# Kernel tuning notes

Measured on AMD Instinct MI355X. Metric: run time of the kernel, lower is better.

## Reference

```python
import jax, jax.numpy as jnp
import numpy as np

WS = (7, 7)        # window size
SHIFT = (3, 3)     # shift size
NUM_HEADS = 12


def _relative_position_index(ws):
    ch, cw = np.arange(ws[0]), np.arange(ws[1])
    coords = np.stack(np.meshgrid(ch, cw, indexing='ij'))          # [2, wh, ww]
    cf = coords.reshape(2, -1)                                     # [2, wh*ww]
    rel = cf[:, :, None] - cf[:, None, :]                          # [2, T, T]
    rel = rel.transpose(1, 2, 0)
    rel[:, :, 0] += ws[0] - 1
    rel[:, :, 1] += ws[1] - 1
    rel[:, :, 0] *= 2 * ws[1] - 1
    return rel.sum(-1)                                             # [T, T]


def _attn_mask(pad_H, pad_W, ws, shift):
    # static construction of the shifted-window mask (numpy, per torch code)
    img = np.zeros((pad_H, pad_W), dtype=np.float32)
    h_slices = ((0, pad_H - ws[0]), (pad_H - ws[0], pad_H - shift[0]), (pad_H - shift[0], pad_H))
    w_slices = ((0, pad_W - ws[1]), (pad_W - ws[1], pad_W - shift[1]), (pad_W - shift[1], pad_W))
    cnt = 0
    for h0, h1 in h_slices:
        for w0, w1 in w_slices:
            img[h0:h1, w0:w1] = cnt
            cnt += 1
    nW = (pad_H // ws[0]) * (pad_W // ws[1])
    m = img.reshape(pad_H // ws[0], ws[0], pad_W // ws[1], ws[1])
    m = m.transpose(0, 2, 1, 3).reshape(nW, ws[0] * ws[1])
    diff = m[:, None, :] - m[:, :, None]
    return np.where(diff != 0, -100.0, 0.0).astype(np.float32)     # [nW, T, T]


def setup_inputs() -> dict:
    key = jax.random.key(0)
    ks = jax.random.split(key, 6)
    dim = 384
    return {
        'x': jax.random.normal(ks[0], (32, 56, 56, dim), dtype=jnp.float32),
        'qkv_weight': jax.random.normal(ks[1], (3 * dim, dim), dtype=jnp.float32) * 0.02,
        'qkv_bias': jax.random.normal(ks[2], (3 * dim,), dtype=jnp.float32) * 0.02,
        'proj_weight': jax.random.normal(ks[3], (dim, dim), dtype=jnp.float32) * 0.02,
        'proj_bias': jax.random.normal(ks[4], (dim,), dtype=jnp.float32) * 0.02,
        'rel_pos_bias_table': jax.random.normal(ks[5], ((2 * WS[0] - 1) * (2 * WS[1] - 1), NUM_HEADS), dtype=jnp.float32) * 0.02,
    }


def reference(x, qkv_weight, qkv_bias, proj_weight, proj_bias, rel_pos_bias_table):
    B, H, W, C = x.shape
    wh, ww = WS
    T = wh * ww
    nh = NUM_HEADS
    dh = C // nh

    pad_b = (wh - H % wh) % wh
    pad_r = (ww - W % ww) % ww
    x = jnp.pad(x, ((0, 0), (0, pad_b), (0, pad_r), (0, 0)))
    pad_H, pad_W = H + pad_b, W + pad_r
    shift = [SHIFT[0] if wh < pad_H else 0, SHIFT[1] if ww < pad_W else 0]

    # relative position bias [1, nh, T, T]
    rpi = _relative_position_index(WS)                               # static int index
    bias = rel_pos_bias_table[jnp.asarray(rpi.reshape(-1))].reshape(T, T, nh)
    bias = jnp.transpose(bias, (2, 0, 1))[None]

    if sum(shift) > 0:
        x = jnp.roll(x, (-shift[0], -shift[1]), axis=(1, 2))

    nH, nW_ = pad_H // wh, pad_W // ww
    num_windows = nH * nW_
    # window partition -> [B*num_windows, T, C]
    xw = x.reshape(B, nH, wh, nW_, ww, C).transpose(0, 1, 3, 2, 4, 5).reshape(B * num_windows, T, C)

    qkv = xw @ qkv_weight.T + qkv_bias                               # [Bn, T, 3C]
    qkv = qkv.reshape(B * num_windows, T, 3, nh, dh).transpose(2, 0, 3, 1, 4)
    q, k, v = qkv[0], qkv[1], qkv[2]                                 # [Bn, nh, T, dh]

    attn = jnp.einsum('bhtd,bhsd->bhts', q * (dh ** -0.5), k) + bias

    if sum(shift) > 0:
        mask = jnp.asarray(_attn_mask(pad_H, pad_W, WS, shift))      # [nW, T, T]
        attn = attn.reshape(B, num_windows, nh, T, T) + mask[None, :, None]
        attn = attn.reshape(B * num_windows, nh, T, T)

    attn = jax.nn.softmax(attn, axis=-1)
    out = jnp.einsum('bhts,bhsd->bhtd', attn, v)                     # [Bn, nh, T, dh]
    out = out.transpose(0, 2, 1, 3).reshape(B * num_windows, T, C)
    out = out @ proj_weight.T + proj_bias

    out = out.reshape(B, nH, nW_, wh, ww, C).transpose(0, 1, 3, 2, 4, 5).reshape(B, pad_H, pad_W, C)
    if sum(shift) > 0:
        out = jnp.roll(out, (shift[0], shift[1]), axis=(1, 2))
    return out[:, :H, :W, :]
```

## Files before the change

### kernel.cpp

```cpp
#include <hip/hip_runtime.h>


typedef __bf16 bf16;
typedef __bf16 bf16x8 __attribute__((ext_vector_type(8)));
typedef __bf16 bf16x4 __attribute__((ext_vector_type(4)));
typedef float f32x4 __attribute__((ext_vector_type(4)));

#define NWIN   2048
#define WHN    24576
#define GTOK   100352
#define QKV_SCALE 0.17677669529663687f

#define QB_OFF 0u
#define KB_OFF 77070336u
#define VB_OFF 154140672u
#define XG_OFF 231211008u
#define BM_OFF 308281344u
#define WQ_OFF 314572800u
#define WP_OFF 315457536u

__device__ inline void gld16(const bf16* g, bf16* l) {
  __builtin_amdgcn_global_load_lds(
      (const __attribute__((address_space(1))) void*)g,
      (__attribute__((address_space(3))) void*)l, 16, 0, 0);
}

__global__ __launch_bounds__(256) void k_prep(
    const float* __restrict__ x, const float* __restrict__ wqkv,
    const float* __restrict__ wproj, const float* __restrict__ table,
    bf16* __restrict__ xg, bf16* __restrict__ wq, bf16* __restrict__ wp,
    bf16* __restrict__ bm) {
  int blk = blockIdx.x;
  if (blk < 18816) {
    int idx = blk * 256 + threadIdx.x;
    int g = idx / 48, cg = idx - g * 48;
    int w = g / 49, t = g - w * 49;
    int b = w >> 6, wi = w & 63;
    int wy = wi >> 3, wx = wi & 7;
    int ty = t / 7, tx = t - ty * 7;
    int sy = wy * 7 + ty + 3; if (sy >= 56) sy -= 56;
    int sx = wx * 7 + tx + 3; if (sx >= 56) sx -= 56;
    const float* src = x + (size_t)((b * 56 + sy) * 56 + sx) * 384 + cg * 8;
    float4 a0 = *(const float4*)src;
    float4 a1 = *(const float4*)(src + 4);
    bf16x8 o;
    o[0] = (bf16)a0.x; o[1] = (bf16)a0.y; o[2] = (bf16)a0.z; o[3] = (bf16)a0.w;
    o[4] = (bf16)a1.x; o[5] = (bf16)a1.y; o[6] = (bf16)a1.z; o[7] = (bf16)a1.w;
    *(bf16x8*)(xg + (size_t)g * 384 + cg * 8) = o;
  } else if (blk < 19104) {
    int idx = (blk - 18816) * 256 + threadIdx.x;
    const float* src; bf16* dst; int off;
    if (idx < 55296) { src = wqkv; dst = wq; off = idx * 8; }
    else             { src = wproj; dst = wp; off = (idx - 55296) * 8; }
    float4 a0 = *(const float4*)(src + off);
    float4 a1 = *(const float4*)(src + off + 4);
    bf16x8 o;
    o[0] = (bf16)a0.x; o[1] = (bf16)a0.y; o[2] = (bf16)a0.z; o[3] = (bf16)a0.w;
    o[4] = (bf16)a1.x; o[5] = (bf16)a1.y; o[6] = (bf16)a1.z; o[7] = (bf16)a1.w;
    *(bf16x8*)(dst + off) = o;
  } else {
    int idx = (blk - 19104) * 256 + threadIdx.x;
    int r = idx & 3;
    int lane = (idx >> 2) & 63;
    int c = (idx >> 8) & 3;
    int ts = (idx >> 10) & 3;
    int comb = idx >> 12;
    int h = comb % 12, wi = comb / 12;
    int i = ts * 16 + ((lane >> 4) << 2) + r;
    int j = c * 16 + (lane & 15);
    float v;
    if (j >= 49) v = -30000.f;
    else if (i >= 49) v = 0.f;
    else {
      int wy = wi >> 3, wx = wi & 7;
      int iy = i / 7, ix = i - iy * 7;
      int jy = j / 7, jx = j - jy * 7;
      int rel = (iy - jy + 6) * 13 + (ix - jx + 6);
      int gyi = wy * 7 + iy, gxi = wx * 7 + ix;
      int gyj = wy * 7 + jy, gxj = wx * 7 + jx;
      int ri = ((gyi < 49) ? 0 : ((gyi < 53) ? 1 : 2)) * 3 +
               ((gxi < 49) ? 0 : ((gxi < 53) ? 1 : 2));
      int rj = ((gyj < 49) ? 0 : ((gyj < 53) ? 1 : 2)) * 3 +
               ((gxj < 49) ? 0 : ((gxj < 53) ? 1 : 2));
      v = table[rel * 12 + h] + ((ri == rj) ? 0.f : -100.f);
    }
    bm[idx] = (bf16)v;
  }
}

__global__ __launch_bounds__(256, 3) void k_qkv(
    const bf16* __restrict__ xg, const bf16* __restrict__ wg,
    const float* __restrict__ bqkv, bf16* __restrict__ qb,
    bf16* __restrict__ kb, bf16* __restrict__ vb) {
  __shared__ __align__(16) bf16 As[128 * 64];
  __shared__ __align__(16) bf16 Bs[128 * 64];

  int tid = threadIdx.x;
  int wv = tid >> 6, lane = tid & 63, l16 = lane & 15, q4 = lane >> 4;
  int wr = wv >> 1, wc = wv & 1;
  int bid = blockIdx.x;
  int xcd = bid & 7, s = bid >> 3;
  int nb = s % 9, mt = s / 9;
  int m0 = (mt * 8 + xcd) * 128;
  int n0 = nb * 128;

  int srow = lane >> 3;
  int scg = lane & 7;

  f32x4 acc[4][4];
#pragma unroll
  for (int a = 0; a < 4; ++a)
#pragma unroll
    for (int b = 0; b < 4; ++b) acc[a][b] = (f32x4){0.f, 0.f, 0.f, 0.f};

  for (int k0 = 0; k0 < 384; k0 += 64) {
    __syncthreads();
#pragma unroll
    for (int st = 0; st < 4; ++st) {
      int row = (wv * 4 + st) * 8 + srow;
      int gc = (scg ^ (row & 7)) * 8;
      gld16(xg + (size_t)(m0 + row) * 384 + k0 + gc, As + (wv * 4 + st) * 512);
      gld16(wg + (size_t)(n0 + row) * 384 + k0 + gc, Bs + (wv * 4 + st) * 512);
    }
    __syncthreads();
#pragma unroll
    for (int kk = 0; kk < 2; ++kk) {
      bf16x8 af[4], bfr[4];
#pragma unroll
      for (int mi = 0; mi < 4; ++mi) {
        int m = wr * 64 + mi * 16 + l16;
        int g = kk * 4 + q4;
        af[mi] = *(const bf16x8*)(As + m * 64 + ((g ^ (m & 7)) * 8));
      }
#pragma unroll
      for (int ci = 0; ci < 4; ++ci) {
        int n = wc * 64 + ci * 16 + l16;
        int g = kk * 4 + q4;
        bfr[ci] = *(const bf16x8*)(Bs + n * 64 + ((g ^ (n & 7)) * 8));
      }
#pragma unroll
      for (int mi = 0; mi < 4; ++mi)
#pragma unroll
        for (int ci = 0; ci < 4; ++ci)
          acc[mi][ci] =
              __builtin_amdgcn_mfma_f32_16x16x32_bf16(af[mi], bfr[ci], acc[mi][ci], 0, 0, 0);
    }
  }

  int which = nb / 3;
  float bias4[4]; int h4[4], d4[4];
#pragma unroll
  for (int ci = 0; ci < 4; ++ci) {
    int n = n0 + wc * 64 + ci * 16 + l16;
    bias4[ci] = bqkv[n];
    int hd = n - which * 384;
    h4[ci] = hd >> 5; d4[ci] = hd & 31;
  }
#pragma unroll
  for (int mi = 0; mi < 4; ++mi) {
#pragma unroll
    for (int r = 0; r < 4; ++r) {
      int mrow = m0 + wr * 64 + mi * 16 + q4 * 4 + r;
      int w = mrow / 49, tt = mrow - w * 49;
      int wb = w * 12;
#pragma unroll
      for (int ci = 0; ci < 4; ++ci) {
        float val = acc[mi][ci][r] + bias4[ci];
        size_t addr = (size_t)((wb + h4[ci]) * 49 + tt) * 32 + d4[ci];
        if (which == 0)
          qb[addr] = (bf16)(val * QKV_SCALE);
        else if (which == 1)
          kb[addr] = (bf16)val;
        else
          vb[addr] = (bf16)val;
      }
    }
  }
}

__global__ __launch_bounds__(256) void k_attn(
    const bf16* __restrict__ qb, const bf16* __restrict__ kb,
    const bf16* __restrict__ vb, const bf16* __restrict__ bm,
    bf16* __restrict__ ab) {
  __shared__ __align__(16) bf16 P[4][16][72];

  int tid = threadIdx.x;
  int wv = tid >> 6, lane = tid & 63, l16 = lane & 15, q4 = lane >> 4;
  int whi = blockIdx.x * 4 + wv;
  int w = whi / 12, h = whi - w * 12;
  int wi = w & 63;

  const bf16* qq = qb + (size_t)whi * 1568;
  const bf16* kk = kb + (size_t)whi * 1568;
  const bf16* vv = vb + (size_t)whi * 1568;
  const bf16* bmb = bm + ((size_t)(wi * 12 + h) << 12);

  bf16x8 kf[4];
#pragma unroll
  for (int c = 0; c < 4; ++c)
    kf[c] = *(const bf16x8*)(kk + (c * 16 + l16) * 32 + q4 * 8);

  bf16x8 vf[2][2];
#pragma unroll
  for (int half = 0; half < 2; ++half)
#pragma unroll
    for (int c2 = 0; c2 < 2; ++c2)
#pragma unroll
      for (int j = 0; j < 8; ++j)
        vf[half][c2][j] = vv[(half * 32 + q4 * 8 + j) * 32 + c2 * 16 + l16];

  const f32x4 zero4 = {0.f, 0.f, 0.f, 0.f};

  for (int ts = 0; ts < 4; ++ts) {
    bf16x8 qf = *(const bf16x8*)(qq + (ts * 16 + l16) * 32 + q4 * 8);
    f32x4 s[4];
#pragma unroll
    for (int c = 0; c < 4; ++c)
      s[c] = __builtin_amdgcn_mfma_f32_16x16x32_bf16(qf, kf[c], zero4, 0, 0, 0);
#pragma unroll
    for (int c = 0; c < 4; ++c) {
      bf16x4 bv = *(const bf16x4*)(bmb + (ts * 4 + c) * 256 + lane * 4);
#pragma unroll
      for (int r = 0; r < 4; ++r) s[c][r] += (float)bv[r];
    }
#pragma unroll
    for (int r = 0; r < 4; ++r) {
      float m = fmaxf(fmaxf(s[0][r], s[1][r]), fmaxf(s[2][r], s[3][r]));
      m = fmaxf(m, __shfl_xor(m, 1));
      m = fmaxf(m, __shfl_xor(m, 2));
      m = fmaxf(m, __shfl_xor(m, 4));
      m = fmaxf(m, __shfl_xor(m, 8));
      float e0 = __expf(s[0][r] - m);
      float e1 = __expf(s[1][r] - m);
      float e2 = __expf(s[2][r] - m);
      float e3 = __expf(s[3][r] - m);
      float sm = e0 + e1 + e2 + e3;
      sm += __shfl_xor(sm, 1);
      sm += __shfl_xor(sm, 2);
      sm += __shfl_xor(sm, 4);
      sm += __shfl_xor(sm, 8);
      float inv = 1.0f / sm;
      int ir = q4 * 4 + r;
      P[wv][ir][l16] = (bf16)(e0 * inv);
      P[wv][ir][16 + l16] = (bf16)(e1 * inv);
      P[wv][ir][32 + l16] = (bf16)(e2 * inv);
      P[wv][ir][48 + l16] = (bf16)(e3 * inv);
    }
    __builtin_amdgcn_wave_barrier();
    bf16x8 p0 = *(const bf16x8*)&P[wv][l16][q4 * 8];
    bf16x8 p1 = *(const bf16x8*)&P[wv][l16][32 + q4 * 8];
    f32x4 o0 = __builtin_amdgcn_mfma_f32_16x16x32_bf16(p0, vf[0][0], zero4, 0, 0, 0);
    o0 = __builtin_amdgcn_mfma_f32_16x16x32_bf16(p1, vf[1][0], o0, 0, 0, 0);
    f32x4 o1 = __builtin_amdgcn_mfma_f32_16x16x32_bf16(p0, vf[0][1], zero4, 0, 0, 0);
    o1 = __builtin_amdgcn_mfma_f32_16x16x32_bf16(p1, vf[1][1], o1, 0, 0, 0);
    __builtin_amdgcn_wave_barrier();
#pragma unroll
    for (int r = 0; r < 4; ++r) {
      int i = ts * 16 + q4 * 4 + r;
      if (i < 49) {
        bf16* dst = ab + (size_t)(w * 49 + i) * 384 + h * 32;
        dst[l16] = (bf16)o0[r];
        dst[16 + l16] = (bf16)o1[r];
      }
    }
  }
}

__global__ __launch_bounds__(256, 3) void k_proj(
    const bf16* __restrict__ ab, const bf16* __restrict__ wp,
    const float* __restrict__ bp, float* __restrict__ out) {
  __shared__ __align__(16) bf16 As[128 * 64];
  __shared__ __align__(16) bf16 Bs[128 * 64];

  int tid = threadIdx.x;
  int wv = tid >> 6, lane = tid & 63, l16 = lane & 15, q4 = lane >> 4;
  int wr = wv >> 1, wc = wv & 1;
  int bid = blockIdx.x;
  int xcd = bid & 7, s = bid >> 3;
  int nb = s % 3, mt = s / 3;
  int m0 = (mt * 8 + xcd) * 128;
  int n0 = nb * 128;

  int srow = lane >> 3;
  int scg = lane & 7;

  f32x4 acc[4][4];
#pragma unroll
  for (int a = 0; a < 4; ++a)
#pragma unroll
    for (int b = 0; b < 4; ++b) acc[a][b] = (f32x4){0.f, 0.f, 0.f, 0.f};

  for (int k0 = 0; k0 < 384; k0 += 64) {
    __syncthreads();
#pragma unroll
    for (int st = 0; st < 4; ++st) {
      int row = (wv * 4 + st) * 8 + srow;
      int gc = (scg ^ (row & 7)) * 8;
      gld16(ab + (size_t)(m0 + row) * 384 + k0 + gc, As + (wv * 4 + st) * 512);
      gld16(wp + (size_t)(n0 + row) * 384 + k0 + gc, Bs + (wv * 4 + st) * 512);
    }
    __syncthreads();
#pragma unroll
    for (int kk = 0; kk < 2; ++kk) {
      bf16x8 af[4], bfr[4];
#pragma unroll
      for (int mi = 0; mi < 4; ++mi) {
        int m = wr * 64 + mi * 16 + l16;
        int g = kk * 4 + q4;
        af[mi] = *(const bf16x8*)(As + m * 64 + ((g ^ (m & 7)) * 8));
      }
#pragma unroll
      for (int ci = 0; ci < 4; ++ci) {
        int n = wc * 64 + ci * 16 + l16;
        int g = kk * 4 + q4;
        bfr[ci] = *(const bf16x8*)(Bs + n * 64 + ((g ^ (n & 7)) * 8));
      }
#pragma unroll
      for (int mi = 0; mi < 4; ++mi)
#pragma unroll
        for (int ci = 0; ci < 4; ++ci)
          acc[mi][ci] =
              __builtin_amdgcn_mfma_f32_16x16x32_bf16(af[mi], bfr[ci], acc[mi][ci], 0, 0, 0);
    }
  }

  float bias4[4]; int col4[4];
#pragma unroll
  for (int ci = 0; ci < 4; ++ci) {
    col4[ci] = n0 + wc * 64 + ci * 16 + l16;
    bias4[ci] = bp[col4[ci]];
  }
#pragma unroll
  for (int mi = 0; mi < 4; ++mi) {
#pragma unroll
    for (int r = 0; r < 4; ++r) {
      int mrow = m0 + wr * 64 + mi * 16 + q4 * 4 + r;
      int w = mrow / 49, t = mrow - w * 49;
      int b = w >> 6, wi = w & 63;
      int wy = wi >> 3, wx = wi & 7;
      int ty = t / 7, tx = t - ty * 7;
      int gy = wy * 7 + ty + 3; if (gy >= 56) gy -= 56;
      int gx = wx * 7 + tx + 3; if (gx >= 56) gx -= 56;
      float* orow = out + (size_t)((b * 56 + gy) * 56 + gx) * 384;
#pragma unroll
      for (int ci = 0; ci < 4; ++ci) orow[col4[ci]] = acc[mi][ci][r] + bias4[ci];
    }
  }
}

extern "C" void kernel_launch(void* const* d_in, const int* in_sizes, int n_in,
                              void* d_out, int out_size, void* d_ws,
                              size_t ws_size, hipStream_t stream) {
  const float* x     = (const float*)d_in[0];
  const float* wqkv  = (const float*)d_in[1];
  const float* bqkv  = (const float*)d_in[2];
  const float* wproj = (const float*)d_in[3];
  const float* bproj = (const float*)d_in[4];
  const float* table = (const float*)d_in[5];
  float* out = (float*)d_out;

  char* ws = (char*)d_ws;
  bf16* qb  = (bf16*)(ws + QB_OFF);
  bf16* kb  = (bf16*)(ws + KB_OFF);
  bf16* vb  = (bf16*)(ws + VB_OFF);
  bf16* xg  = (bf16*)(ws + XG_OFF);
  bf16* ab  = (bf16*)(ws + XG_OFF);
  bf16* bmb = (bf16*)(ws + BM_OFF);
  bf16* wqg = (bf16*)(ws + WQ_OFF);
  bf16* wpg = (bf16*)(ws + WP_OFF);

  k_prep<<<dim3(31392), dim3(256), 0, stream>>>(x, wqkv, wproj, table,
                                                xg, wqg, wpg, bmb);
  k_qkv<<<dim3(7056), dim3(256), 0, stream>>>(xg, wqg, bqkv, qb, kb, vb);
  k_attn<<<dim3(6144), dim3(256), 0, stream>>>(qb, kb, vb, bmb, ab);
  k_proj<<<dim3(2352), dim3(256), 0, stream>>>(ab, wpg, bproj, out);
}
```

Before: 526.7 us.

## Fuse QKV GEMM, window attention and projection into one per-window kernel

Replaces the three kernels for the QKV GEMM, attention and projection with a single kernel that processes one window per block. The padded 64-token window input is staged in LDS, and per-head Q/K/V and the attention output stay on chip, so the large Q/K/V and attention-output round trips through global memory disappear. The prep kernel now pads each window to 64 rows with zeros. In exchange each block uses about 120KB of LDS (occupancy 1), reads weights directly from global/L2 without LDS tiling, and does GEMM work on 15 padding rows per window.

```diff
diff --git a/kernel.cpp b/kernel.cpp
--- a/kernel.cpp
+++ b/kernel.cpp
@@ -6,18 +6,12 @@
 typedef __bf16 bf16x4 __attribute__((ext_vector_type(4)));
 typedef float f32x4 __attribute__((ext_vector_type(4)));
 
-#define NWIN   2048
-#define WHN    24576
-#define GTOK   100352
 #define QKV_SCALE 0.17677669529663687f
 
-#define QB_OFF 0u
-#define KB_OFF 77070336u
-#define VB_OFF 154140672u
-#define XG_OFF 231211008u
-#define BM_OFF 308281344u
-#define WQ_OFF 314572800u
-#define WP_OFF 315457536u
+#define XG_OFF 0u
+#define BM_OFF 100663296u
+#define WQ_OFF 106954752u
+#define WP_OFF 107839488u
 
 __device__ inline void gld16(const bf16* g, bf16* l) {
   __builtin_amdgcn_global_load_lds(
@@ -31,24 +25,28 @@
     bf16* __restrict__ xg, bf16* __restrict__ wq, bf16* __restrict__ wp,
     bf16* __restrict__ bm) {
   int blk = blockIdx.x;
-  if (blk < 18816) {
+  if (blk < 24576) {
     int idx = blk * 256 + threadIdx.x;
     int g = idx / 48, cg = idx - g * 48;
-    int w = g / 49, t = g - w * 49;
-    int b = w >> 6, wi = w & 63;
-    int wy = wi >> 3, wx = wi & 7;
-    int ty = t / 7, tx = t - ty * 7;
-    int sy = wy * 7 + ty + 3; if (sy >= 56) sy -= 56;
-    int sx = wx * 7 + tx + 3; if (sx >= 56) sx -= 56;
-    const float* src = x + (size_t)((b * 56 + sy) * 56 + sx) * 384 + cg * 8;
-    float4 a0 = *(const float4*)src;
-    float4 a1 = *(const float4*)(src + 4);
+    int w = g >> 6, t = g & 63;
     bf16x8 o;
-    o[0] = (bf16)a0.x; o[1] = (bf16)a0.y; o[2] = (bf16)a0.z; o[3] = (bf16)a0.w;
-    o[4] = (bf16)a1.x; o[5] = (bf16)a1.y; o[6] = (bf16)a1.z; o[7] = (bf16)a1.w;
+#pragma unroll
+    for (int j = 0; j < 8; ++j) o[j] = (bf16)0.f;
+    if (t < 49) {
+      int b = w >> 6, wi = w & 63;
+      int wy = wi >> 3, wx = wi & 7;
+      int ty = t / 7, tx = t - ty * 7;
+      int sy = wy * 7 + ty + 3; if (sy >= 56) sy -= 56;
+      int sx = wx * 7 + tx + 3; if (sx >= 56) sx -= 56;
+      const float* src = x + (size_t)((b * 56 + sy) * 56 + sx) * 384 + cg * 8;
+      float4 a0 = *(const float4*)src;
+      float4 a1 = *(const float4*)(src + 4);
+      o[0] = (bf16)a0.x; o[1] = (bf16)a0.y; o[2] = (bf16)a0.z; o[3] = (bf16)a0.w;
+      o[4] = (bf16)a1.x; o[5] = (bf16)a1.y; o[6] = (bf16)a1.z; o[7] = (bf16)a1.w;
+    }
     *(bf16x8*)(xg + (size_t)g * 384 + cg * 8) = o;
-  } else if (blk < 19104) {
-    int idx = (blk - 18816) * 256 + threadIdx.x;
+  } else if (blk < 24864) {
+    int idx = (blk - 24576) * 256 + threadIdx.x;
     const float* src; bf16* dst; int off;
     if (idx < 55296) { src = wqkv; dst = wq; off = idx * 8; }
     else             { src = wproj; dst = wp; off = (idx - 55296) * 8; }
@@ -59,7 +57,7 @@
     o[4] = (bf16)a1.x; o[5] = (bf16)a1.y; o[6] = (bf16)a1.z; o[7] = (bf16)a1.w;
     *(bf16x8*)(dst + off) = o;
   } else {
-    int idx = (blk - 19104) * 256 + threadIdx.x;
+    int idx = (blk - 24864) * 256 + threadIdx.x;
     int r = idx & 3;
     int lane = (idx >> 2) & 63;
     int c = (idx >> 8) & 3;
@@ -88,262 +86,214 @@
   }
 }
 
-__global__ __launch_bounds__(256, 3) void k_qkv(
-    const bf16* __restrict__ xg, const bf16* __restrict__ wg,
-    const float* __restrict__ bqkv, bf16* __restrict__ qb,
-    bf16* __restrict__ kb, bf16* __restrict__ vb) {
-  __shared__ __align__(16) bf16 As[128 * 64];
-  __shared__ __align__(16) bf16 Bs[128 * 64];
+__global__ __launch_bounds__(256, 1) void k_fused(
+    const bf16* __restrict__ xg, const bf16* __restrict__ wq,
+    const float* __restrict__ bqkv, const bf16* __restrict__ bm,
+    const bf16* __restrict__ wp, const float* __restrict__ bp,
+    float* __restrict__ out) {
+  __shared__ __align__(16) bf16 X[64 * 384];
+  __shared__ __align__(16) bf16 QKV[4][3][64 * 32];
+  __shared__ __align__(16) bf16 AB[64 * 384];
+  __shared__ __align__(16) bf16 P[4][16][72];
 
   int tid = threadIdx.x;
   int wv = tid >> 6, lane = tid & 63, l16 = lane & 15, q4 = lane >> 4;
-  int wr = wv >> 1, wc = wv & 1;
-  int bid = blockIdx.x;
-  int xcd = bid & 7, s = bid >> 3;
-  int nb = s % 9, mt = s / 9;
-  int m0 = (mt * 8 + xcd) * 128;
-  int n0 = nb * 128;
-
-  int srow = lane >> 3;
-  int scg = lane & 7;
-
-  f32x4 acc[4][4];
-#pragma unroll
-  for (int a = 0; a < 4; ++a)
-#pragma unroll
-    for (int b = 0; b < 4; ++b) acc[a][b] = (f32x4){0.f, 0.f, 0.f, 0.f};
-
-  for (int k0 = 0; k0 < 384; k0 += 64) {
-    __syncthreads();
-#pragma unroll
-    for (int st = 0; st < 4; ++st) {
-      int row = (wv * 4 + st) * 8 + srow;
-      int gc = (scg ^ (row & 7)) * 8;
-      gld16(xg + (size_t)(m0 + row) * 384 + k0 + gc, As + (wv * 4 + st) * 512);
-      gld16(wg + (size_t)(n0 + row) * 384 + k0 + gc, Bs + (wv * 4 + st) * 512);
-    }
-    __syncthreads();
-#pragma unroll
-    for (int kk = 0; kk < 2; ++kk) {
-      bf16x8 af[4], bfr[4];
+  int w = blockIdx.x;
+  int wi = w & 63;
+
+  const bf16* xw = xg + (size_t)w * (64 * 384);
+#pragma unroll
+  for (int it = 0; it < 12; ++it) {
+    int cb = it * 256 + wv * 64;
+    int d = cb + lane;
+    int row = d / 48, gcol = d - row * 48;
+    gld16(xw + row * 384 + ((gcol ^ (row & 7)) << 3), X + cb * 8);
+  }
+  __syncthreads();
+
+  const f32x4 zero4 = {0.f, 0.f, 0.f, 0.f};
+
+  for (int hr = 0; hr < 3; ++hr) {
+    int h = wv * 3 + hr;
+
+    f32x4 acc[4][6];
+#pragma unroll
+    for (int a = 0; a < 4; ++a)
+#pragma unroll
+      for (int b = 0; b < 6; ++b) acc[a][b] = zero4;
+
+    const bf16* wrow[6];
+#pragma unroll
+    for (int ci = 0; ci < 6; ++ci) {
+      int part = ci >> 1, cc = ci & 1;
+      wrow[ci] = wq + (size_t)(part * 384 + h * 32 + cc * 16 + l16) * 384 + q4 * 8;
+    }
+#pragma unroll
+    for (int ks = 0; ks < 12; ++ks) {
+      bf16x8 af[4], bfr[6];
 #pragma unroll
       for (int mi = 0; mi < 4; ++mi) {
-        int m = wr * 64 + mi * 16 + l16;
-        int g = kk * 4 + q4;
-        af[mi] = *(const bf16x8*)(As + m * 64 + ((g ^ (m & 7)) * 8));
-      }
-#pragma unroll
-      for (int ci = 0; ci < 4; ++ci) {
-        int n = wc * 64 + ci * 16 + l16;
-        int g = kk * 4 + q4;
-        bfr[ci] = *(const bf16x8*)(Bs + n * 64 + ((g ^ (n & 7)) * 8));
-      }
+        int m = mi * 16 + l16;
+        int g = ks * 4 + q4;
+        af[mi] = *(const bf16x8*)(X + m * 384 + ((g ^ (m & 7)) << 3));
+      }
+#pragma unroll
+      for (int ci = 0; ci < 6; ++ci)
+        bfr[ci] = *(const bf16x8*)(wrow[ci] + ks * 32);
+      __builtin_amdgcn_s_setprio(1);
 #pragma unroll
       for (int mi = 0; mi < 4; ++mi)
 #pragma unroll
-        for (int ci = 0; ci < 4; ++ci)
-          acc[mi][ci] =
-              __builtin_amdgcn_mfma_f32_16x16x32_bf16(af[mi], bfr[ci], acc[mi][ci], 0, 0, 0);
+        for (int ci = 0; ci < 6; ++ci)
+          acc[mi][ci] = __builtin_amdgcn_mfma_f32_16x16x32_bf16(
+              af[mi], bfr[ci], acc[mi][ci], 0, 0, 0);
+      __builtin_amdgcn_s_setprio(0);
+    }
+#pragma unroll
+    for (int ci = 0; ci < 6; ++ci) {
+      int part = ci >> 1, cc = ci & 1;
+      float bias = bqkv[part * 384 + h * 32 + cc * 16 + l16];
+      float scl = (part == 0) ? QKV_SCALE : 1.0f;
+      bf16* dst = &QKV[wv][part][cc * 16 + l16];
+#pragma unroll
+      for (int mi = 0; mi < 4; ++mi)
+#pragma unroll
+        for (int r = 0; r < 4; ++r)
+          dst[(mi * 16 + q4 * 4 + r) * 32] = (bf16)((acc[mi][ci][r] + bias) * scl);
+    }
+    __builtin_amdgcn_wave_barrier();
+
+    const bf16* qqb = &QKV[wv][0][0];
+    const bf16* kkb = &QKV[wv][1][0];
+    const bf16* vvb = &QKV[wv][2][0];
+    const bf16* bmh = bm + ((size_t)(wi * 12 + h) << 12);
+
+    bf16x8 kf[4];
+#pragma unroll
+    for (int c = 0; c < 4; ++c)
+      kf[c] = *(const bf16x8*)(kkb + (c * 16 + l16) * 32 + q4 * 8);
+    bf16x8 vf[2][2];
+#pragma unroll
+    for (int half = 0; half < 2; ++half)
+#pragma unroll
+      for (int c2 = 0; c2 < 2; ++c2)
+#pragma unroll
+        for (int j = 0; j < 8; ++j)
+          vf[half][c2][j] = vvb[(half * 32 + q4 * 8 + j) * 32 + c2 * 16 + l16];
+
+    for (int ts = 0; ts < 4; ++ts) {
+      bf16x8 qf = *(const bf16x8*)(qqb + (ts * 16 + l16) * 32 + q4 * 8);
+      f32x4 s[4];
+#pragma unroll
+      for (int c = 0; c < 4; ++c)
+        s[c] = __builtin_amdgcn_mfma_f32_16x16x32_bf16(qf, kf[c], zero4, 0, 0, 0);
+#pragma unroll
+      for (int c = 0; c < 4; ++c) {
+        bf16x4 bv = *(const bf16x4*)(bmh + (ts * 4 + c) * 256 + lane * 4);
+#pragma unroll
+        for (int r = 0; r < 4; ++r) s[c][r] += (float)bv[r];
+      }
+#pragma unroll
+      for (int r = 0; r < 4; ++r) {
+        float m = fmaxf(fmaxf(s[0][r], s[1][r]), fmaxf(s[2][r], s[3][r]));
+        m = fmaxf(m, __shfl_xor(m, 1));
+        m = fmaxf(m, __shfl_xor(m, 2));
+        m = fmaxf(m, __shfl_xor(m, 4));
+        m = fmaxf(m, __shfl_xor(m, 8));
+        float e0 = __expf(s[0][r] - m);
+        float e1 = __expf(s[1][r] - m);
+        float e2 = __expf(s[2][r] - m);
+        float e3 = __expf(s[3][r] - m);
+        float sm = e0 + e1 + e2 + e3;
+        sm += __shfl_xor(sm, 1);
+        sm += __shfl_xor(sm, 2);
+        sm += __shfl_xor(sm, 4);
+        sm += __shfl_xor(sm, 8);
+        float inv = 1.0f / sm;
+        int ir = q4 * 4 + r;
+        P[wv][ir][l16] = (bf16)(e0 * inv);
+        P[wv][ir][16 + l16] = (bf16)(e1 * inv);
+        P[wv][ir][32 + l16] = (bf16)(e2 * inv);
+        P[wv][ir][48 + l16] = (bf16)(e3 * inv);
+      }
+      __builtin_amdgcn_wave_barrier();
+      bf16x8 p0 = *(const bf16x8*)&P[wv][l16][q4 * 8];
+      bf16x8 p1 = *(const bf16x8*)&P[wv][l16][32 + q4 * 8];
+      f32x4 o0 = __builtin_amdgcn_mfma_f32_16x16x32_bf16(p0, vf[0][0], zero4, 0, 0, 0);
+      o0 = __builtin_amdgcn_mfma_f32_16x16x32_bf16(p1, vf[1][0], o0, 0, 0, 0);
+      f32x4 o1 = __builtin_amdgcn_mfma_f32_16x16x32_bf16(p0, vf[0][1], zero4, 0, 0, 0);
+      o1 = __builtin_amdgcn_mfma_f32_16x16x32_bf16(p1, vf[1][1], o1, 0, 0, 0);
+      __builtin_amdgcn_wave_barrier();
+#pragma unroll
+      for (int r = 0; r < 4; ++r) {
+        int i = ts * 16 + q4 * 4 + r;
+        int isw = i & 7;
+        int c0 = h * 32 + l16;
+        AB[i * 384 + (((c0 >> 3) ^ isw) << 3) + (c0 & 7)] = (bf16)o0[r];
+        int c1 = h * 32 + 16 + l16;
+        AB[i * 384 + (((c1 >> 3) ^ isw) << 3) + (c1 & 7)] = (bf16)o1[r];
+      }
     }
   }
 
-  int which = nb / 3;
-  float bias4[4]; int h4[4], d4[4];
-#pragma unroll
-  for (int ci = 0; ci < 4; ++ci) {
-    int n = n0 + wc * 64 + ci * 16 + l16;
-    bias4[ci] = bqkv[n];
-    int hd = n - which * 384;
-    h4[ci] = hd >> 5; d4[ci] = hd & 31;
-  }
-#pragma unroll
-  for (int mi = 0; mi < 4; ++mi) {
-#pragma unroll
-    for (int r = 0; r < 4; ++r) {
-      int mrow = m0 + wr * 64 + mi * 16 + q4 * 4 + r;
-      int w = mrow / 49, tt = mrow - w * 49;
-      int wb = w * 12;
-#pragma unroll
-      for (int ci = 0; ci < 4; ++ci) {
-        float val = acc[mi][ci][r] + bias4[ci];
-        size_t addr = (size_t)((wb + h4[ci]) * 49 + tt) * 32 + d4[ci];
-        if (which == 0)
-          qb[addr] = (bf16)(val * QKV_SCALE);
-        else if (which == 1)
-          kb[addr] = (bf16)val;
-        else
-          vb[addr] = (bf16)val;
-      }
-    }
-  }
-}
-
-__global__ __launch_bounds__(256) void k_attn(
-    const bf16* __restrict__ qb, const bf16* __restrict__ kb,
-    const bf16* __restrict__ vb, const bf16* __restrict__ bm,
-    bf16* __restrict__ ab) {
-  __shared__ __align__(16) bf16 P[4][16][72];
-
-  int tid = threadIdx.x;
-  int wv = tid >> 6, lane = tid & 63, l16 = lane & 15, q4 = lane >> 4;
-  int whi = blockIdx.x * 4 + wv;
-  int w = whi / 12, h = whi - w * 12;
-  int wi = w & 63;
-
-  const bf16* qq = qb + (size_t)whi * 1568;
-  const bf16* kk = kb + (size_t)whi * 1568;
-  const bf16* vv = vb + (size_t)whi * 1568;
-  const bf16* bmb = bm + ((size_t)(wi * 12 + h) << 12);
-
-  bf16x8 kf[4];
-#pragma unroll
-  for (int c = 0; c < 4; ++c)
-    kf[c] = *(const bf16x8*)(kk + (c * 16 + l16) * 32 + q4 * 8);
-
-  bf16x8 vf[2][2];
-#pragma unroll
-  for (int half = 0; half < 2; ++half)
-#pragma unroll
-    for (int c2 = 0; c2 < 2; ++c2)
-#pragma unroll
-      for (int j = 0; j < 8; ++j)
-        vf[half][c2][j] = vv[(half * 32 + q4 * 8 + j) * 32 + c2 * 16 + l16];
-
-  const f32x4 zero4 = {0.f, 0.f, 0.f, 0.f};
-
-  for (int ts = 0; ts < 4; ++ts) {
-    bf16x8 qf = *(const bf16x8*)(qq + (ts * 16 + l16) * 32 + q4 * 8);
-    f32x4 s[4];
-#pragma unroll
-    for (int c = 0; c < 4; ++c)
-      s[c] = __builtin_amdgcn_mfma_f32_16x16x32_bf16(qf, kf[c], zero4, 0, 0, 0);
-#pragma unroll
-    for (int c = 0; c < 4; ++c) {
-      bf16x4 bv = *(const bf16x4*)(bmb + (ts * 4 + c) * 256 + lane * 4);
-#pragma unroll
-      for (int r = 0; r < 4; ++r) s[c][r] += (float)bv[r];
-    }
-#pragma unroll
-    for (int r = 0; r < 4; ++r) {
-      float m = fmaxf(fmaxf(s[0][r], s[1][r]), fmaxf(s[2][r], s[3][r]));
-      m = fmaxf(m, __shfl_xor(m, 1));
-      m = fmaxf(m, __shfl_xor(m, 2));
-      m = fmaxf(m, __shfl_xor(m, 4));
-      m = fmaxf(m, __shfl_xor(m, 8));
-      float e0 = __expf(s[0][r] - m);
-      float e1 = __expf(s[1][r] - m);
-      float e2 = __expf(s[2][r] - m);
-      float e3 = __expf(s[3][r] - m);
-      float sm = e0 + e1 + e2 + e3;
-      sm += __shfl_xor(sm, 1);
-      sm += __shfl_xor(sm, 2);
-      sm += __shfl_xor(sm, 4);
-      sm += __shfl_xor(sm, 8);
-      float inv = 1.0f / sm;
-      int ir = q4 * 4 + r;
-      P[wv][ir][l16] = (bf16)(e0 * inv);
-      P[wv][ir][16 + l16] = (bf16)(e1 * inv);
-      P[wv][ir][32 + l16] = (bf16)(e2 * inv);
-      P[wv][ir][48 + l16] = (bf16)(e3 * inv);
-    }
-    __builtin_amdgcn_wave_barrier();
-    bf16x8 p0 = *(const bf16x8*)&P[wv][l16][q4 * 8];
-    bf16x8 p1 = *(const bf16x8*)&P[wv][l16][32 + q4 * 8];
-    f32x4 o0 = __builtin_amdgcn_mfma_f32_16x16x32_bf16(p0, vf[0][0], zero4, 0, 0, 0);
-    o0 = __builtin_amdgcn_mfma_f32_16x16x32_bf16(p1, vf[1][0], o0, 0, 0, 0);
-    f32x4 o1 = __builtin_amdgcn_mfma_f32_16x16x32_bf16(p0, vf[0][1], zero4, 0, 0, 0);
-    o1 = __builtin_amdgcn_mfma_f32_16x16x32_bf16(p1, vf[1][1], o1, 0, 0, 0);
-    __builtin_amdgcn_wave_barrier();
-#pragma unroll
-    for (int r = 0; r < 4; ++r) {
-      int i = ts * 16 + q4 * 4 + r;
-      if (i < 49) {
-        bf16* dst = ab + (size_t)(w * 49 + i) * 384 + h * 32;
-        dst[l16] = (bf16)o0[r];
-        dst[16 + l16] = (bf16)o1[r];
-      }
-    }
-  }
-}
-
-__global__ __launch_bounds__(256, 3) void k_proj(
-    const bf16* __restrict__ ab, const bf16* __restrict__ wp,
-    const float* __restrict__ bp, float* __restrict__ out) {
-  __shared__ __align__(16) bf16 As[128 * 64];
-  __shared__ __align__(16) bf16 Bs[128 * 64];
-
-  int tid = threadIdx.x;
-  int wv = tid >> 6, lane = tid & 63, l16 = lane & 15, q4 = lane >> 4;
-  int wr = wv >> 1, wc = wv & 1;
-  int bid = blockIdx.x;
-  int xcd = bid & 7, s = bid >> 3;
-  int nb = s % 3, mt = s / 3;
-  int m0 = (mt * 8 + xcd) * 128;
-  int n0 = nb * 128;
-
-  int srow = lane >> 3;
-  int scg = lane & 7;
-
-  f32x4 acc[4][4];
-#pragma unroll
-  for (int a = 0; a < 4; ++a)
-#pragma unroll
-    for (int b = 0; b < 4; ++b) acc[a][b] = (f32x4){0.f, 0.f, 0.f, 0.f};
-
-  for (int k0 = 0; k0 < 384; k0 += 64) {
-    __syncthreads();
-#pragma unroll
-    for (int st = 0; st < 4; ++st) {
-      int row = (wv * 4 + st) * 8 + srow;
-      int gc = (scg ^ (row & 7)) * 8;
-      gld16(ab + (size_t)(m0 + row) * 384 + k0 + gc, As + (wv * 4 + st) * 512);
-      gld16(wp + (size_t)(n0 + row) * 384 + k0 + gc, Bs + (wv * 4 + st) * 512);
-    }
-    __syncthreads();
-#pragma unroll
-    for (int kk = 0; kk < 2; ++kk) {
-      bf16x8 af[4], bfr[4];
+  __syncthreads();
+
+  {
+    f32x4 pacc[4][6];
+#pragma unroll
+    for (int a = 0; a < 4; ++a)
+#pragma unroll
+      for (int b = 0; b < 6; ++b) pacc[a][b] = zero4;
+
+    const bf16* wrow[6];
+#pragma unroll
+    for (int ci = 0; ci < 6; ++ci)
+      wrow[ci] = wp + (size_t)(wv * 96 + ci * 16 + l16) * 384 + q4 * 8;
+#pragma unroll
+    for (int ks = 0; ks < 12; ++ks) {
+      bf16x8 af[4], bfr[6];
 #pragma unroll
       for (int mi = 0; mi < 4; ++mi) {
-        int m = wr * 64 + mi * 16 + l16;
-        int g = kk * 4 + q4;
-        af[mi] = *(const bf16x8*)(As + m * 64 + ((g ^ (m & 7)) * 8));
-      }
-#pragma unroll
-      for (int ci = 0; ci < 4; ++ci) {
-        int n = wc * 64 + ci * 16 + l16;
-        int g = kk * 4 + q4;
-        bfr[ci] = *(const bf16x8*)(Bs + n * 64 + ((g ^ (n & 7)) * 8));
-      }
+        int m = mi * 16 + l16;
+        int g = ks * 4 + q4;
+        af[mi] = *(const bf16x8*)(AB + m * 384 + ((g ^ (m & 7)) << 3));
+      }
+#pragma unroll
+      for (int ci = 0; ci < 6; ++ci)
+        bfr[ci] = *(const bf16x8*)(wrow[ci] + ks * 32);
+      __builtin_amdgcn_s_setprio(1);
 #pragma unroll
       for (int mi = 0; mi < 4; ++mi)
 #pragma unroll
-        for (int ci = 0; ci < 4; ++ci)
-          acc[mi][ci] =
-              __builtin_amdgcn_mfma_f32_16x16x32_bf16(af[mi], bfr[ci], acc[mi][ci], 0, 0, 0);
-    }
-  }
-
-  float bias4[4]; int col4[4];
-#pragma unroll
-  for (int ci = 0; ci < 4; ++ci) {
-    col4[ci] = n0 + wc * 64 + ci * 16 + l16;
-    bias4[ci] = bp[col4[ci]];
-  }
-#pragma unroll
-  for (int mi = 0; mi < 4; ++mi) {
-#pragma unroll
-    for (int r = 0; r < 4; ++r) {
-      int mrow = m0 + wr * 64 + mi * 16 + q4 * 4 + r;
-      int w = mrow / 49, t = mrow - w * 49;
-      int b = w >> 6, wi = w & 63;
-      int wy = wi >> 3, wx = wi & 7;
-      int ty = t / 7, tx = t - ty * 7;
-      int gy = wy * 7 + ty + 3; if (gy >= 56) gy -= 56;
-      int gx = wx * 7 + tx + 3; if (gx >= 56) gx -= 56;
-      float* orow = out + (size_t)((b * 56 + gy) * 56 + gx) * 384;
-#pragma unroll
-      for (int ci = 0; ci < 4; ++ci) orow[col4[ci]] = acc[mi][ci][r] + bias4[ci];
+        for (int ci = 0; ci < 6; ++ci)
+          pacc[mi][ci] = __builtin_amdgcn_mfma_f32_16x16x32_bf16(
+              af[mi], bfr[ci], pacc[mi][ci], 0, 0, 0);
+      __builtin_amdgcn_s_setprio(0);
+    }
+
+    int b = w >> 6;
+    int wy = wi >> 3, wx = wi & 7;
+    float bias6[6]; int col6[6];
+#pragma unroll
+    for (int ci = 0; ci < 6; ++ci) {
+      col6[ci] = wv * 96 + ci * 16 + l16;
+      bias6[ci] = bp[col6[ci]];
+    }
+#pragma unroll
+    for (int mi = 0; mi < 4; ++mi) {
+#pragma unroll
+      for (int r = 0; r < 4; ++r) {
+        int t = mi * 16 + q4 * 4 + r;
+        if (t < 49) {
+          int ty = t / 7, tx = t - ty * 7;
+          int gy = wy * 7 + ty + 3; if (gy >= 56) gy -= 56;
+          int gx = wx * 7 + tx + 3; if (gx >= 56) gx -= 56;
+          float* orow = out + (size_t)((b * 56 + gy) * 56 + gx) * 384;
+#pragma unroll
+          for (int ci = 0; ci < 6; ++ci)
+            orow[col6[ci]] = pacc[mi][ci][r] + bias6[ci];
+        }
+      }
     }
   }
 }
@@ -360,18 +310,13 @@
   float* out = (float*)d_out;
 
   char* ws = (char*)d_ws;
-  bf16* qb  = (bf16*)(ws + QB_OFF);
-  bf16* kb  = (bf16*)(ws + KB_OFF);
-  bf16* vb  = (bf16*)(ws + VB_OFF);
   bf16* xg  = (bf16*)(ws + XG_OFF);
-  bf16* ab  = (bf16*)(ws + XG_OFF);
   bf16* bmb = (bf16*)(ws + BM_OFF);
   bf16* wqg = (bf16*)(ws + WQ_OFF);
   bf16* wpg = (bf16*)(ws + WP_OFF);
 
-  k_prep<<<dim3(31392), dim3(256), 0, stream>>>(x, wqkv, wproj, table,
+  k_prep<<<dim3(37152), dim3(256), 0, stream>>>(x, wqkv, wproj, table,
                                                 xg, wqg, wpg, bmb);
-  k_qkv<<<dim3(7056), dim3(256), 0, stream>>>(xg, wqg, bqkv, qb, kb, vb);
-  k_attn<<<dim3(6144), dim3(256), 0, stream>>>(qb, kb, vb, bmb, ab);
-  k_proj<<<dim3(2352), dim3(256), 0, stream>>>(ab, wpg, bproj, out);
+  k_fused<<<dim3(2048), dim3(256), 0, stream>>>(xg, wqg, bqkv, bmb,
+                                                wpg, bproj, out);
 }
```

Result: slower. 708.6 us (+34.5%).

## Fuse shifted-window gather and bf16 conversion of x into QKV GEMM

Applied to the files above, without the earlier changes.

The separate pre-pass that gathered x into shifted-window order and converted it to bf16 is gone. The QKV GEMM now loads the fp32 rows of x directly into registers, computing the cyclic-shift source address per row, converts them to bf16 and stores them swizzled into shared memory. This removes a full write and re-read of a bf16 copy of the activations. In exchange, each column-block CTA re-reads fp32 x, twice the bytes of the old bf16 copy, relying on L2 reuse across the nine N-tiles scheduled on the same XCD. The A tile also moves from asynchronous global-to-LDS loads to synchronous register staging.

```diff
diff --git a/kernel.cpp b/kernel.cpp
--- a/kernel.cpp
+++ b/kernel.cpp
@@ -6,15 +6,12 @@
 typedef __bf16 bf16x4 __attribute__((ext_vector_type(4)));
 typedef float f32x4 __attribute__((ext_vector_type(4)));
 
-#define NWIN   2048
-#define WHN    24576
-#define GTOK   100352
 #define QKV_SCALE 0.17677669529663687f
 
 #define QB_OFF 0u
 #define KB_OFF 77070336u
 #define VB_OFF 154140672u
-#define XG_OFF 231211008u
+#define AB_OFF 231211008u
 #define BM_OFF 308281344u
 #define WQ_OFF 314572800u
 #define WP_OFF 315457536u
@@ -26,29 +23,12 @@
 }
 
 __global__ __launch_bounds__(256) void k_prep(
-    const float* __restrict__ x, const float* __restrict__ wqkv,
-    const float* __restrict__ wproj, const float* __restrict__ table,
-    bf16* __restrict__ xg, bf16* __restrict__ wq, bf16* __restrict__ wp,
-    bf16* __restrict__ bm) {
+    const float* __restrict__ wqkv, const float* __restrict__ wproj,
+    const float* __restrict__ table, bf16* __restrict__ wq,
+    bf16* __restrict__ wp, bf16* __restrict__ bm) {
   int blk = blockIdx.x;
-  if (blk < 18816) {
+  if (blk < 288) {
     int idx = blk * 256 + threadIdx.x;
-    int g = idx / 48, cg = idx - g * 48;
-    int w = g / 49, t = g - w * 49;
-    int b = w >> 6, wi = w & 63;
-    int wy = wi >> 3, wx = wi & 7;
-    int ty = t / 7, tx = t - ty * 7;
-    int sy = wy * 7 + ty + 3; if (sy >= 56) sy -= 56;
-    int sx = wx * 7 + tx + 3; if (sx >= 56) sx -= 56;
-    const float* src = x + (size_t)((b * 56 + sy) * 56 + sx) * 384 + cg * 8;
-    float4 a0 = *(const float4*)src;
-    float4 a1 = *(const float4*)(src + 4);
-    bf16x8 o;
-    o[0] = (bf16)a0.x; o[1] = (bf16)a0.y; o[2] = (bf16)a0.z; o[3] = (bf16)a0.w;
-    o[4] = (bf16)a1.x; o[5] = (bf16)a1.y; o[6] = (bf16)a1.z; o[7] = (bf16)a1.w;
-    *(bf16x8*)(xg + (size_t)g * 384 + cg * 8) = o;
-  } else if (blk < 19104) {
-    int idx = (blk - 18816) * 256 + threadIdx.x;
     const float* src; bf16* dst; int off;
     if (idx < 55296) { src = wqkv; dst = wq; off = idx * 8; }
     else             { src = wproj; dst = wp; off = (idx - 55296) * 8; }
@@ -59,7 +39,7 @@
     o[4] = (bf16)a1.x; o[5] = (bf16)a1.y; o[6] = (bf16)a1.z; o[7] = (bf16)a1.w;
     *(bf16x8*)(dst + off) = o;
   } else {
-    int idx = (blk - 19104) * 256 + threadIdx.x;
+    int idx = (blk - 288) * 256 + threadIdx.x;
     int r = idx & 3;
     int lane = (idx >> 2) & 63;
     int c = (idx >> 8) & 3;
@@ -89,7 +69,7 @@
 }
 
 __global__ __launch_bounds__(256, 3) void k_qkv(
-    const bf16* __restrict__ xg, const bf16* __restrict__ wg,
+    const float* __restrict__ x, const bf16* __restrict__ wg,
     const float* __restrict__ bqkv, bf16* __restrict__ qb,
     bf16* __restrict__ kb, bf16* __restrict__ vb) {
   __shared__ __align__(16) bf16 As[128 * 64];
@@ -107,6 +87,18 @@
   int srow = lane >> 3;
   int scg = lane & 7;
 
+  int arow = tid >> 1, ahalf = tid & 1;
+  int mrow = m0 + arow;
+  int wA = mrow / 49, tA = mrow - wA * 49;
+  int bA = wA >> 6, wiA = wA & 63;
+  int wyA = wiA >> 3, wxA = wiA & 7;
+  int tyA = tA / 7, txA = tA - tyA * 7;
+  int syA = wyA * 7 + tyA + 3; if (syA >= 56) syA -= 56;
+  int sxA = wxA * 7 + txA + 3; if (sxA >= 56) sxA -= 56;
+  const float* xrow = x + (size_t)((bA * 56 + syA) * 56 + sxA) * 384 + ahalf * 32;
+  bf16* adst = As + arow * 64;
+  int ar7 = arow & 7;
+
   f32x4 acc[4][4];
 #pragma unroll
   for (int a = 0; a < 4; ++a)
@@ -114,13 +106,25 @@
     for (int b = 0; b < 4; ++b) acc[a][b] = (f32x4){0.f, 0.f, 0.f, 0.f};
 
   for (int k0 = 0; k0 < 384; k0 += 64) {
+    float4 f[8];
+#pragma unroll
+    for (int j = 0; j < 8; ++j) f[j] = *(const float4*)(xrow + k0 + j * 4);
     __syncthreads();
 #pragma unroll
     for (int st = 0; st < 4; ++st) {
       int row = (wv * 4 + st) * 8 + srow;
       int gc = (scg ^ (row & 7)) * 8;
-      gld16(xg + (size_t)(m0 + row) * 384 + k0 + gc, As + (wv * 4 + st) * 512);
       gld16(wg + (size_t)(n0 + row) * 384 + k0 + gc, Bs + (wv * 4 + st) * 512);
+    }
+#pragma unroll
+    for (int j2 = 0; j2 < 4; ++j2) {
+      bf16x8 o;
+      o[0] = (bf16)f[2 * j2].x;     o[1] = (bf16)f[2 * j2].y;
+      o[2] = (bf16)f[2 * j2].z;     o[3] = (bf16)f[2 * j2].w;
+      o[4] = (bf16)f[2 * j2 + 1].x; o[5] = (bf16)f[2 * j2 + 1].y;
+      o[6] = (bf16)f[2 * j2 + 1].z; o[7] = (bf16)f[2 * j2 + 1].w;
+      int g = ahalf * 4 + j2;
+      *(bf16x8*)(adst + ((g ^ ar7) << 3)) = o;
     }
     __syncthreads();
 #pragma unroll
@@ -160,8 +164,8 @@
   for (int mi = 0; mi < 4; ++mi) {
 #pragma unroll
     for (int r = 0; r < 4; ++r) {
-      int mrow = m0 + wr * 64 + mi * 16 + q4 * 4 + r;
-      int w = mrow / 49, tt = mrow - w * 49;
+      int mr = m0 + wr * 64 + mi * 16 + q4 * 4 + r;
+      int w = mr / 49, tt = mr - w * 49;
       int wb = w * 12;
 #pragma unroll
       for (int ci = 0; ci < 4; ++ci) {
@@ -334,8 +338,8 @@
   for (int mi = 0; mi < 4; ++mi) {
 #pragma unroll
     for (int r = 0; r < 4; ++r) {
-      int mrow = m0 + wr * 64 + mi * 16 + q4 * 4 + r;
-      int w = mrow / 49, t = mrow - w * 49;
+      int mr = m0 + wr * 64 + mi * 16 + q4 * 4 + r;
+      int w = mr / 49, t = mr - w * 49;
       int b = w >> 6, wi = w & 63;
       int wy = wi >> 3, wx = wi & 7;
       int ty = t / 7, tx = t - ty * 7;
@@ -363,15 +367,14 @@
   bf16* qb  = (bf16*)(ws + QB_OFF);
   bf16* kb  = (bf16*)(ws + KB_OFF);
   bf16* vb  = (bf16*)(ws + VB_OFF);
-  bf16* xg  = (bf16*)(ws + XG_OFF);
-  bf16* ab  = (bf16*)(ws + XG_OFF);
+  bf16* ab  = (bf16*)(ws + AB_OFF);
   bf16* bmb = (bf16*)(ws + BM_OFF);
   bf16* wqg = (bf16*)(ws + WQ_OFF);
   bf16* wpg = (bf16*)(ws + WP_OFF);
 
-  k_prep<<<dim3(31392), dim3(256), 0, stream>>>(x, wqkv, wproj, table,
-                                                xg, wqg, wpg, bmb);
-  k_qkv<<<dim3(7056), dim3(256), 0, stream>>>(xg, wqg, bqkv, qb, kb, vb);
+  k_prep<<<dim3(12576), dim3(256), 0, stream>>>(wqkv, wproj, table,
+                                                wqg, wpg, bmb);
+  k_qkv<<<dim3(7056), dim3(256), 0, stream>>>(x, wqg, bqkv, qb, kb, vb);
   k_attn<<<dim3(6144), dim3(256), 0, stream>>>(qb, kb, vb, bmb, ab);
   k_proj<<<dim3(2352), dim3(256), 0, stream>>>(ab, wpg, bproj, out);
 }
```

Measured after the change: 581.5 us. 1.1x slower.
